# Optimization experiments

Measured on AMD Instinct MI355X. Metric: run time of the kernel, lower is better.

Reference implementation:

```python
import jax, jax.numpy as jnp
import numpy as np

NUM_EXPERTS = 8
HIDDEN = 1024
FFN = 2048
TOKENS = 2048


def setup_inputs() -> dict:
    key = jax.random.key(0)
    k_x, k_idx, k_w1, k_w2 = jax.random.split(key, 4)
    scale = 0.02
    x = jax.random.normal(k_x, (TOKENS, HIDDEN), dtype=jnp.float32)
    expert_indices = jax.random.randint(k_idx, (TOKENS,), 0, NUM_EXPERTS, dtype=jnp.int64)
    W1 = jax.random.normal(k_w1, (NUM_EXPERTS, HIDDEN, FFN), dtype=jnp.float32) * scale
    b1 = jnp.zeros((NUM_EXPERTS, FFN), dtype=jnp.float32)
    W2 = jax.random.normal(k_w2, (NUM_EXPERTS, FFN, HIDDEN), dtype=jnp.float32) * scale
    b2 = jnp.zeros((NUM_EXPERTS, HIDDEN), dtype=jnp.float32)
    return {"x": x, "expert_indices": expert_indices, "W1": W1, "b1": b1, "W2": W2, "b2": b2}


def reference(x, expert_indices, W1, b1, W2, b2):
    # Each token routed to one expert's MLP: Linear -> GELU(exact) -> Linear.
    # Dropout is identity in eval mode. Loop is over the small fixed expert set.
    out = jnp.zeros_like(x)
    for e in range(NUM_EXPERTS):
        h = jax.nn.gelu(x @ W1[e] + b1[e], approximate=False)  # [T, FFN]
        y = h @ W2[e] + b2[e]                                   # [T, H]
        mask = (expert_indices == e)[:, None]
        out = out + jnp.where(mask, y, 0.0)
    return out
```

## Files before the change

kernel.cpp:

```cpp
#include <hip/hip_runtime.h>

#define T_TOK 2048
#define HID   1024
#define FFN   2048
#define NEXP  8
#define MAX_SLOTS 40

typedef __attribute__((ext_vector_type(8))) short bf16x8;
typedef __attribute__((ext_vector_type(4))) float f32x4;

__device__ __forceinline__ short f2bf(float f) {
    unsigned u = __builtin_bit_cast(unsigned, f);
    u = (u + 0x7fffu + ((u >> 16) & 1u)) >> 16;
    return (short)u;
}

__device__ __forceinline__ float gelu_exact(float x) {
    return 0.5f * x * (1.0f + erff(x * 0.70710678118654752f));
}

__device__ __forceinline__ void async_cp16(const short* g, short* l) {
    __builtin_amdgcn_global_load_lds(
        (const __attribute__((address_space(1))) unsigned int*)g,
        (__attribute__((address_space(3))) unsigned int*)l, 16, 0, 0);
}

__global__ __launch_bounds__(256) void prep_kernel(
        const float* __restrict__ x, const int* __restrict__ idx,
        const float* __restrict__ b2,
        short* __restrict__ xb, float* __restrict__ out,
        int* __restrict__ offs, int* __restrict__ cnts,
        int* __restrict__ tokl,
        int* __restrict__ slot_e, int* __restrict__ slot_t0) {
    int bx = blockIdx.x;
    int tid = threadIdx.x;
    if (bx < 1024) {
        int i = (bx * 256 + tid) * 8;
        float4 v0 = *(const float4*)(x + i);
        float4 v1 = *(const float4*)(x + i + 4);
        bf16x8 r = {f2bf(v0.x), f2bf(v0.y), f2bf(v0.z), f2bf(v0.w),
                    f2bf(v1.x), f2bf(v1.y), f2bf(v1.z), f2bf(v1.w)};
        *(bf16x8*)(xb + i) = r;
    } else if (bx < 1024 + T_TOK) {
        int t = bx - 1024;
        int e = idx[t];
        ((float4*)(out + (size_t)t * HID))[tid] =
            ((const float4*)(b2 + (size_t)e * HID))[tid];
    } else {
        __shared__ int c[NEXP], cur[NEXP], o[NEXP];
        if (tid < NEXP) { c[tid] = 0; cur[tid] = 0; }
        __syncthreads();
        for (int t = tid; t < T_TOK; t += 256) atomicAdd(&c[idx[t]], 1);
        __syncthreads();
        if (tid == 0) {
            int s = 0;
            for (int e = 0; e < NEXP; e++) { o[e] = s; s += c[e]; }
            int ns = 0;
            for (int e = 0; e < NEXP; e++)
                for (int t0 = 0; t0 < c[e]; t0 += 64) {
                    slot_e[ns] = e; slot_t0[ns] = t0; ns++;
                }
            for (; ns < MAX_SLOTS; ns++) slot_e[ns] = -1;
        }
        __syncthreads();
        if (tid < NEXP) { offs[tid] = o[tid]; cnts[tid] = c[tid]; }
        for (int t = tid; t < T_TOK; t += 256) {
            int e = idx[t];
            int p = o[e] + atomicAdd(&cur[e], 1);
            tokl[p] = t;
        }
    }
}

__global__ __launch_bounds__(256) void wtrans_kernel(
        const float* __restrict__ W1, const float* __restrict__ W2,
        short* __restrict__ W1T, short* __restrict__ W2T) {
    int z = blockIdx.z;
    const float* W; short* WT; int K, N, e;
    if (z < NEXP) { W = W1; WT = W1T; K = HID; N = FFN; e = z; }
    else          { W = W2; WT = W2T; K = FFN; N = HID; e = z - NEXP; }
    int n0 = blockIdx.x * 64, k0 = blockIdx.y * 64;
    if (n0 >= N || k0 >= K) return;
    const float* We = W + (size_t)e * K * N;
    short* WTe = WT + (size_t)e * N * K;
    __shared__ short Ts[64][72];
    int tid = threadIdx.x;
#pragma unroll
    for (int i = 0; i < 4; i++) {
        int c = tid + i * 256;
        int k = c >> 4, n4 = (c & 15) * 4;
        float4 v = *(const float4*)(We + (size_t)(k0 + k) * N + n0 + n4);
        short s0 = f2bf(v.x), s1 = f2bf(v.y), s2 = f2bf(v.z), s3 = f2bf(v.w);
        int ck = k >> 3, kj = k & 7;
        Ts[n4 + 0][((ck ^ (((n4 + 0) >> 3) & 7)) << 3) + kj] = s0;
        Ts[n4 + 1][((ck ^ (((n4 + 1) >> 3) & 7)) << 3) + kj] = s1;
        Ts[n4 + 2][((ck ^ (((n4 + 2) >> 3) & 7)) << 3) + kj] = s2;
        Ts[n4 + 3][((ck ^ (((n4 + 3) >> 3) & 7)) << 3) + kj] = s3;
    }
    __syncthreads();
#pragma unroll
    for (int i = 0; i < 2; i++) {
        int c = tid + i * 256;
        int n = c >> 3, ck = c & 7;
        bf16x8 v = *(const bf16x8*)&Ts[n][(ck ^ ((n >> 3) & 7)) << 3];
        *(bf16x8*)(WTe + (size_t)(n0 + n) * K + k0 + ck * 8) = v;
    }
}

__global__ __launch_bounds__(256) void gemm1_kernel(
        const short* __restrict__ xb, const short* __restrict__ W1T,
        const float* __restrict__ b1,
        const int* __restrict__ offs, const int* __restrict__ cnts,
        const int* __restrict__ tokl,
        const int* __restrict__ slot_e, const int* __restrict__ slot_t0,
        short* __restrict__ hg) {
    int s = blockIdx.y;
    int e = slot_e[s];
    if (e < 0) return;
    int t0 = slot_t0[s];
    int count = cnts[e];
    int off = offs[e];
    int n0 = blockIdx.x * 64;

    __shared__ short As[64 * 32];
    __shared__ short Bs[64 * 32];
    __shared__ int stok[64];

    int tid = threadIdx.x;
    if (tid < 64) {
        int p = t0 + tid;
        stok[tid] = tokl[off + (p < count ? p : count - 1)];
    }
    __syncthreads();

    int w = tid >> 6, lane = tid & 63, l15 = lane & 15, quad = lane >> 4;
    int wm = (w >> 1) * 32, wn = (w & 1) * 32;

    int srow = w * 16 + (lane >> 2);
    int schunk = (lane & 3) * 8;
    const short* gA = xb + (size_t)stok[srow] * HID + schunk;
    const short* gB = W1T + (size_t)e * FFN * HID + (size_t)(n0 + srow) * HID + schunk;
    short* lA = &As[w * 16 * 32];
    short* lB = &Bs[w * 16 * 32];

    f32x4 acc[2][2];
#pragma unroll
    for (int i = 0; i < 2; i++)
#pragma unroll
        for (int j = 0; j < 2; j++) acc[i][j] = (f32x4){0.f, 0.f, 0.f, 0.f};

    for (int kt = 0; kt < HID / 32; kt++) {
        async_cp16(gA + kt * 32, lA);
        async_cp16(gB + kt * 32, lB);
        __syncthreads();
        bf16x8 a0 = *(const bf16x8*)&As[(wm + l15) * 32 + quad * 8];
        bf16x8 a1 = *(const bf16x8*)&As[(wm + 16 + l15) * 32 + quad * 8];
        bf16x8 b0 = *(const bf16x8*)&Bs[(wn + l15) * 32 + quad * 8];
        bf16x8 b1v = *(const bf16x8*)&Bs[(wn + 16 + l15) * 32 + quad * 8];
        acc[0][0] = __builtin_amdgcn_mfma_f32_16x16x32_bf16(a0, b0, acc[0][0], 0, 0, 0);
        acc[0][1] = __builtin_amdgcn_mfma_f32_16x16x32_bf16(a0, b1v, acc[0][1], 0, 0, 0);
        acc[1][0] = __builtin_amdgcn_mfma_f32_16x16x32_bf16(a1, b0, acc[1][0], 0, 0, 0);
        acc[1][1] = __builtin_amdgcn_mfma_f32_16x16x32_bf16(a1, b1v, acc[1][1], 0, 0, 0);
        __syncthreads();
    }

#pragma unroll
    for (int mt = 0; mt < 2; mt++) {
        int rbase = wm + mt * 16 + quad * 4;
#pragma unroll
        for (int nt = 0; nt < 2; nt++) {
            int coln = n0 + wn + nt * 16 + l15;
            float bb = b1[e * FFN + coln];
#pragma unroll
            for (int r = 0; r < 4; r++) {
                int p = t0 + rbase + r;
                if (p < count) {
                    float hv = gelu_exact(acc[mt][nt][r] + bb);
                    hg[(size_t)(off + p) * FFN + coln] = f2bf(hv);
                }
            }
        }
    }
}

__global__ __launch_bounds__(256) void gemm2_kernel(
        const short* __restrict__ hg, const short* __restrict__ W2T,
        const int* __restrict__ offs, const int* __restrict__ cnts,
        const int* __restrict__ tokl,
        const int* __restrict__ slot_e, const int* __restrict__ slot_t0,
        float* __restrict__ out) {
    int s = blockIdx.y;
    int e = slot_e[s];
    if (e < 0) return;
    int t0 = slot_t0[s];
    int ks = blockIdx.z;
    int count = cnts[e];
    int off = offs[e];
    int n0 = blockIdx.x * 64;
    int kbase = ks * (FFN / 4);

    __shared__ short As[64 * 32];
    __shared__ short Bs[64 * 32];

    int tid = threadIdx.x;
    int w = tid >> 6, lane = tid & 63, l15 = lane & 15, quad = lane >> 4;
    int wm = (w >> 1) * 32, wn = (w & 1) * 32;

    int srow = w * 16 + (lane >> 2);
    int schunk = (lane & 3) * 8;
    int grow = off + (t0 + srow < count ? t0 + srow : count - 1);
    const short* gA = hg + (size_t)grow * FFN + kbase + schunk;
    const short* gB = W2T + (size_t)e * HID * FFN + (size_t)(n0 + srow) * FFN + kbase + schunk;
    short* lA = &As[w * 16 * 32];
    short* lB = &Bs[w * 16 * 32];

    f32x4 acc[2][2];
#pragma unroll
    for (int i = 0; i < 2; i++)
#pragma unroll
        for (int j = 0; j < 2; j++) acc[i][j] = (f32x4){0.f, 0.f, 0.f, 0.f};

    for (int kt = 0; kt < FFN / 4 / 32; kt++) {
        async_cp16(gA + kt * 32, lA);
        async_cp16(gB + kt * 32, lB);
        __syncthreads();
        bf16x8 a0 = *(const bf16x8*)&As[(wm + l15) * 32 + quad * 8];
        bf16x8 a1 = *(const bf16x8*)&As[(wm + 16 + l15) * 32 + quad * 8];
        bf16x8 b0 = *(const bf16x8*)&Bs[(wn + l15) * 32 + quad * 8];
        bf16x8 b1v = *(const bf16x8*)&Bs[(wn + 16 + l15) * 32 + quad * 8];
        acc[0][0] = __builtin_amdgcn_mfma_f32_16x16x32_bf16(a0, b0, acc[0][0], 0, 0, 0);
        acc[0][1] = __builtin_amdgcn_mfma_f32_16x16x32_bf16(a0, b1v, acc[0][1], 0, 0, 0);
        acc[1][0] = __builtin_amdgcn_mfma_f32_16x16x32_bf16(a1, b0, acc[1][0], 0, 0, 0);
        acc[1][1] = __builtin_amdgcn_mfma_f32_16x16x32_bf16(a1, b1v, acc[1][1], 0, 0, 0);
        __syncthreads();
    }

#pragma unroll
    for (int mt = 0; mt < 2; mt++) {
        int rbase = wm + mt * 16 + quad * 4;
#pragma unroll
        for (int nt = 0; nt < 2; nt++) {
            int coln = n0 + wn + nt * 16 + l15;
#pragma unroll
            for (int r = 0; r < 4; r++) {
                int p = t0 + rbase + r;
                if (p < count) {
                    int tok = tokl[off + p];
                    atomicAdd(out + (size_t)tok * HID + coln, acc[mt][nt][r]);
                }
            }
        }
    }
}

extern "C" void kernel_launch(void* const* d_in, const int* in_sizes, int n_in,
                              void* d_out, int out_size, void* d_ws, size_t ws_size,
                              hipStream_t stream) {
    const float* x   = (const float*)d_in[0];
    const int*   idx = (const int*)d_in[1];
    const float* W1  = (const float*)d_in[2];
    const float* b1  = (const float*)d_in[3];
    const float* W2  = (const float*)d_in[4];
    const float* b2  = (const float*)d_in[5];
    float* out = (float*)d_out;

    const size_t META = 32768;
    int*   offs    = (int*)d_ws;
    int*   cnts    = offs + 8;
    int*   tokl    = offs + 16;
    int*   slot_e  = offs + 16 + T_TOK;
    int*   slot_t0 = slot_e + MAX_SLOTS;
    char*  base    = (char*)d_ws + META;
    short* xb  = (short*)base;
    short* hg  = (short*)(base + (size_t)T_TOK * HID * 2);
    short* W1T = (short*)(base + (size_t)T_TOK * HID * 2 + (size_t)T_TOK * FFN * 2);
    short* W2T = W1T + (size_t)NEXP * FFN * HID;

    prep_kernel<<<1024 + T_TOK + 1, 256, 0, stream>>>(
        x, idx, b2, xb, out, offs, cnts, tokl, slot_e, slot_t0);
    wtrans_kernel<<<dim3(32, 32, 16), 256, 0, stream>>>(W1, W2, W1T, W2T);

    gemm1_kernel<<<dim3(FFN / 64, MAX_SLOTS), 256, 0, stream>>>(
        xb, W1T, b1, offs, cnts, tokl, slot_e, slot_t0, hg);
    gemm2_kernel<<<dim3(HID / 64, MAX_SLOTS, 4), 256, 0, stream>>>(
        hg, W2T, offs, cnts, tokl, slot_e, slot_t0, out);
}
```

Baseline: 255.0 us.

## Fuse weight transpose into prep kernel and enlarge GEMM tiles with panel layout

The separate weight transpose kernel is folded into the prep kernel. It now writes W1/W2 as bf16 in a k-panel-blocked layout (64 k by 128 n panels), built with register transposes instead of LDS. Both GEMMs move to 64x128 tiles with a 64-wide k step, contiguous B-panel loads and an XOR-rotated A layout in LDS. GEMM2 uses 2 k-splits instead of 4. The goal is to cut launch count, barrier and load overhead per MFMA, and atomic traffic. The cost is fewer blocks in flight and higher register pressure.

```diff
diff --git a/kernel.cpp b/kernel.cpp
--- a/kernel.cpp
+++ b/kernel.cpp
@@ -25,24 +25,63 @@
         (__attribute__((address_space(3))) unsigned int*)l, 16, 0, 0);
 }
 
+__device__ __forceinline__ void wtrans_body(
+        const float* __restrict__ W, short* __restrict__ WT,
+        int K, int N, int e, int kblk, int nblk) {
+    int tid = threadIdx.x;
+    int w = tid >> 6, l = tid & 63;
+    int kb = kblk * 32 + w * 8;
+    int n4 = nblk * 256 + l * 4;
+    const float* src = W + (size_t)e * K * N + (size_t)kb * N + n4;
+    float4 v[8];
+#pragma unroll
+    for (int r = 0; r < 8; r++)
+        v[r] = *(const float4*)(src + (size_t)r * N);
+    int kpanel = kb >> 6;
+    int kc = (kb >> 3) & 7;
+    int npanel = n4 >> 7;
+    int n_in = n4 & 127;
+    int kpanels = K >> 6;
+    short* dst = WT + (size_t)e * K * N
+               + ((size_t)npanel * kpanels + kpanel) * 8192
+               + kc * 1024 + n_in * 8;
+#pragma unroll
+    for (int j = 0; j < 4; j++) {
+        bf16x8 o = {f2bf(((const float*)&v[0])[j]), f2bf(((const float*)&v[1])[j]),
+                    f2bf(((const float*)&v[2])[j]), f2bf(((const float*)&v[3])[j]),
+                    f2bf(((const float*)&v[4])[j]), f2bf(((const float*)&v[5])[j]),
+                    f2bf(((const float*)&v[6])[j]), f2bf(((const float*)&v[7])[j])};
+        *(bf16x8*)(dst + j * 8) = o;
+    }
+}
+
 __global__ __launch_bounds__(256) void prep_kernel(
         const float* __restrict__ x, const int* __restrict__ idx,
         const float* __restrict__ b2,
+        const float* __restrict__ W1, const float* __restrict__ W2,
         short* __restrict__ xb, float* __restrict__ out,
+        short* __restrict__ W1T, short* __restrict__ W2T,
         int* __restrict__ offs, int* __restrict__ cnts,
         int* __restrict__ tokl,
         int* __restrict__ slot_e, int* __restrict__ slot_t0) {
     int bx = blockIdx.x;
     int tid = threadIdx.x;
-    if (bx < 1024) {
-        int i = (bx * 256 + tid) * 8;
+    if (bx < 2048) {
+        int e = bx >> 8, rem = bx & 255;
+        wtrans_body(W1, W1T, HID, FFN, e, rem & 31, rem >> 5);
+    } else if (bx < 4096) {
+        int b = bx - 2048;
+        int e = b >> 8, rem = b & 255;
+        wtrans_body(W2, W2T, FFN, HID, e, rem & 63, rem >> 6);
+    } else if (bx < 5120) {
+        int i = ((bx - 4096) * 256 + tid) * 8;
         float4 v0 = *(const float4*)(x + i);
         float4 v1 = *(const float4*)(x + i + 4);
         bf16x8 r = {f2bf(v0.x), f2bf(v0.y), f2bf(v0.z), f2bf(v0.w),
                     f2bf(v1.x), f2bf(v1.y), f2bf(v1.z), f2bf(v1.w)};
         *(bf16x8*)(xb + i) = r;
-    } else if (bx < 1024 + T_TOK) {
-        int t = bx - 1024;
+    } else if (bx < 7168) {
+        int t = bx - 5120;
         int e = idx[t];
         ((float4*)(out + (size_t)t * HID))[tid] =
             ((const float4*)(b2 + (size_t)e * HID))[tid];
@@ -69,41 +108,6 @@
             int p = o[e] + atomicAdd(&cur[e], 1);
             tokl[p] = t;
         }
-    }
-}
-
-__global__ __launch_bounds__(256) void wtrans_kernel(
-        const float* __restrict__ W1, const float* __restrict__ W2,
-        short* __restrict__ W1T, short* __restrict__ W2T) {
-    int z = blockIdx.z;
-    const float* W; short* WT; int K, N, e;
-    if (z < NEXP) { W = W1; WT = W1T; K = HID; N = FFN; e = z; }
-    else          { W = W2; WT = W2T; K = FFN; N = HID; e = z - NEXP; }
-    int n0 = blockIdx.x * 64, k0 = blockIdx.y * 64;
-    if (n0 >= N || k0 >= K) return;
-    const float* We = W + (size_t)e * K * N;
-    short* WTe = WT + (size_t)e * N * K;
-    __shared__ short Ts[64][72];
-    int tid = threadIdx.x;
-#pragma unroll
-    for (int i = 0; i < 4; i++) {
-        int c = tid + i * 256;
-        int k = c >> 4, n4 = (c & 15) * 4;
-        float4 v = *(const float4*)(We + (size_t)(k0 + k) * N + n0 + n4);
-        short s0 = f2bf(v.x), s1 = f2bf(v.y), s2 = f2bf(v.z), s3 = f2bf(v.w);
-        int ck = k >> 3, kj = k & 7;
-        Ts[n4 + 0][((ck ^ (((n4 + 0) >> 3) & 7)) << 3) + kj] = s0;
-        Ts[n4 + 1][((ck ^ (((n4 + 1) >> 3) & 7)) << 3) + kj] = s1;
-        Ts[n4 + 2][((ck ^ (((n4 + 2) >> 3) & 7)) << 3) + kj] = s2;
-        Ts[n4 + 3][((ck ^ (((n4 + 3) >> 3) & 7)) << 3) + kj] = s3;
-    }
-    __syncthreads();
-#pragma unroll
-    for (int i = 0; i < 2; i++) {
-        int c = tid + i * 256;
-        int n = c >> 3, ck = c & 7;
-        bf16x8 v = *(const bf16x8*)&Ts[n][(ck ^ ((n >> 3) & 7)) << 3];
-        *(bf16x8*)(WTe + (size_t)(n0 + n) * K + k0 + ck * 8) = v;
     }
 }
 
@@ -117,13 +121,11 @@
     int s = blockIdx.y;
     int e = slot_e[s];
     if (e < 0) return;
-    int t0 = slot_t0[s];
-    int count = cnts[e];
-    int off = offs[e];
-    int n0 = blockIdx.x * 64;
-
-    __shared__ short As[64 * 32];
-    __shared__ short Bs[64 * 32];
+    int t0 = slot_t0[s], count = cnts[e], off = offs[e];
+    int n0 = blockIdx.x * 128;
+
+    __shared__ short As[64 * 64];
+    __shared__ short Bs[8 * 128 * 8];
     __shared__ int stok[64];
 
     int tid = threadIdx.x;
@@ -133,51 +135,79 @@
     }
     __syncthreads();
 
-    int w = tid >> 6, lane = tid & 63, l15 = lane & 15, quad = lane >> 4;
-    int wm = (w >> 1) * 32, wn = (w & 1) * 32;
-
-    int srow = w * 16 + (lane >> 2);
-    int schunk = (lane & 3) * 8;
-    const short* gA = xb + (size_t)stok[srow] * HID + schunk;
-    const short* gB = W1T + (size_t)e * FFN * HID + (size_t)(n0 + srow) * HID + schunk;
-    short* lA = &As[w * 16 * 32];
-    short* lB = &Bs[w * 16 * 32];
-
-    f32x4 acc[2][2];
+    int w = tid >> 6, l = tid & 63, l15 = l & 15, quad = l >> 4;
+    int wm = (w >> 1) * 32, wn = (w & 1) * 64;
+
+    int m0 = w * 16 + (l >> 3), m1 = m0 + 8;
+    int cs = l & 7;
+    int c0 = (cs - m0) & 7, c1 = (cs - m1) & 7;
+    const short* gA0 = xb + (size_t)stok[m0] * HID + c0 * 8;
+    const short* gA1 = xb + (size_t)stok[m1] * HID + c1 * 8;
+    short* lA0 = As + w * 1024 + l * 8;
+    short* lA1 = lA0 + 512;
+
+    const short* Bpan = W1T + (size_t)e * (FFN * HID)
+                      + (size_t)(n0 >> 7) * ((HID >> 6) * 8192);
+    int bo0 = (2 * w) * 1024 + l * 8;
+    int bo1 = bo0 + 1024;
+    int bo2 = bo0 + 512;
+    int bo3 = bo1 + 512;
+
+    f32x4 acc[2][4];
 #pragma unroll
     for (int i = 0; i < 2; i++)
 #pragma unroll
-        for (int j = 0; j < 2; j++) acc[i][j] = (f32x4){0.f, 0.f, 0.f, 0.f};
-
-    for (int kt = 0; kt < HID / 32; kt++) {
-        async_cp16(gA + kt * 32, lA);
-        async_cp16(gB + kt * 32, lB);
-        __syncthreads();
-        bf16x8 a0 = *(const bf16x8*)&As[(wm + l15) * 32 + quad * 8];
-        bf16x8 a1 = *(const bf16x8*)&As[(wm + 16 + l15) * 32 + quad * 8];
-        bf16x8 b0 = *(const bf16x8*)&Bs[(wn + l15) * 32 + quad * 8];
-        bf16x8 b1v = *(const bf16x8*)&Bs[(wn + 16 + l15) * 32 + quad * 8];
-        acc[0][0] = __builtin_amdgcn_mfma_f32_16x16x32_bf16(a0, b0, acc[0][0], 0, 0, 0);
-        acc[0][1] = __builtin_amdgcn_mfma_f32_16x16x32_bf16(a0, b1v, acc[0][1], 0, 0, 0);
-        acc[1][0] = __builtin_amdgcn_mfma_f32_16x16x32_bf16(a1, b0, acc[1][0], 0, 0, 0);
-        acc[1][1] = __builtin_amdgcn_mfma_f32_16x16x32_bf16(a1, b1v, acc[1][1], 0, 0, 0);
-        __syncthreads();
-    }
-
+        for (int j = 0; j < 4; j++) acc[i][j] = (f32x4){0.f, 0.f, 0.f, 0.f};
+
+    for (int kt = 0; kt < HID / 64; kt++) {
+        const short* bp = Bpan + kt * 8192;
+        async_cp16(gA0, lA0);
+        async_cp16(gA1, lA1);
+        async_cp16(bp + bo0, Bs + bo0);
+        async_cp16(bp + bo1, Bs + bo1);
+        async_cp16(bp + bo2, Bs + bo2);
+        async_cp16(bp + bo3, Bs + bo3);
+        gA0 += 64; gA1 += 64;
+        __syncthreads();
+        bf16x8 a[2][2], b[2][4];
+#pragma unroll
+        for (int kk = 0; kk < 2; kk++) {
+#pragma unroll
+            for (int mt = 0; mt < 2; mt++) {
+                int m = wm + mt * 16 + l15;
+                a[kk][mt] = *(const bf16x8*)&As[m * 64 + (((kk * 4 + quad) + m) & 7) * 8];
+            }
+#pragma unroll
+            for (int nt = 0; nt < 4; nt++) {
+                int n = wn + nt * 16 + l15;
+                b[kk][nt] = *(const bf16x8*)&Bs[(kk * 4 + quad) * 1024 + n * 8];
+            }
+        }
+#pragma unroll
+        for (int kk = 0; kk < 2; kk++)
+#pragma unroll
+            for (int mt = 0; mt < 2; mt++)
+#pragma unroll
+                for (int nt = 0; nt < 4; nt++)
+                    acc[mt][nt] = __builtin_amdgcn_mfma_f32_16x16x32_bf16(
+                        a[kk][mt], b[kk][nt], acc[mt][nt], 0, 0, 0);
+        __syncthreads();
+    }
+
+    const float* b1e = b1 + e * FFN + n0;
 #pragma unroll
     for (int mt = 0; mt < 2; mt++) {
         int rbase = wm + mt * 16 + quad * 4;
 #pragma unroll
-        for (int nt = 0; nt < 2; nt++) {
-            int coln = n0 + wn + nt * 16 + l15;
-            float bb = b1[e * FFN + coln];
+        for (int nt = 0; nt < 4; nt++) {
+            int coln = wn + nt * 16 + l15;
+            float bb = b1e[coln];
 #pragma unroll
             for (int r = 0; r < 4; r++) {
                 int p = t0 + rbase + r;
-                if (p < count) {
-                    float hv = gelu_exact(acc[mt][nt][r] + bb);
-                    hg[(size_t)(off + p) * FFN + coln] = f2bf(hv);
-                }
+                if (p < count)
+                    hg[(size_t)(off + p) * FFN + n0 + coln] =
+                        f2bf(gelu_exact(acc[mt][nt][r] + bb));
             }
         }
     }
@@ -192,46 +222,73 @@
     int s = blockIdx.y;
     int e = slot_e[s];
     if (e < 0) return;
-    int t0 = slot_t0[s];
+    int t0 = slot_t0[s], count = cnts[e], off = offs[e];
     int ks = blockIdx.z;
-    int count = cnts[e];
-    int off = offs[e];
-    int n0 = blockIdx.x * 64;
-    int kbase = ks * (FFN / 4);
-
-    __shared__ short As[64 * 32];
-    __shared__ short Bs[64 * 32];
+    int n0 = blockIdx.x * 128;
+
+    __shared__ short As[64 * 64];
+    __shared__ short Bs[8 * 128 * 8];
 
     int tid = threadIdx.x;
-    int w = tid >> 6, lane = tid & 63, l15 = lane & 15, quad = lane >> 4;
-    int wm = (w >> 1) * 32, wn = (w & 1) * 32;
-
-    int srow = w * 16 + (lane >> 2);
-    int schunk = (lane & 3) * 8;
-    int grow = off + (t0 + srow < count ? t0 + srow : count - 1);
-    const short* gA = hg + (size_t)grow * FFN + kbase + schunk;
-    const short* gB = W2T + (size_t)e * HID * FFN + (size_t)(n0 + srow) * FFN + kbase + schunk;
-    short* lA = &As[w * 16 * 32];
-    short* lB = &Bs[w * 16 * 32];
-
-    f32x4 acc[2][2];
+    int w = tid >> 6, l = tid & 63, l15 = l & 15, quad = l >> 4;
+    int wm = (w >> 1) * 32, wn = (w & 1) * 64;
+
+    int m0 = w * 16 + (l >> 3), m1 = m0 + 8;
+    int cs = l & 7;
+    int c0 = (cs - m0) & 7, c1 = (cs - m1) & 7;
+    int g0 = off + (t0 + m0 < count ? t0 + m0 : count - 1);
+    int g1 = off + (t0 + m1 < count ? t0 + m1 : count - 1);
+    const short* gA0 = hg + (size_t)g0 * FFN + ks * 1024 + c0 * 8;
+    const short* gA1 = hg + (size_t)g1 * FFN + ks * 1024 + c1 * 8;
+    short* lA0 = As + w * 1024 + l * 8;
+    short* lA1 = lA0 + 512;
+
+    const short* Bpan = W2T + (size_t)e * (FFN * HID)
+                      + (size_t)(n0 >> 7) * ((FFN >> 6) * 8192)
+                      + (size_t)ks * 16 * 8192;
+    int bo0 = (2 * w) * 1024 + l * 8;
+    int bo1 = bo0 + 1024;
+    int bo2 = bo0 + 512;
+    int bo3 = bo1 + 512;
+
+    f32x4 acc[2][4];
 #pragma unroll
     for (int i = 0; i < 2; i++)
 #pragma unroll
-        for (int j = 0; j < 2; j++) acc[i][j] = (f32x4){0.f, 0.f, 0.f, 0.f};
-
-    for (int kt = 0; kt < FFN / 4 / 32; kt++) {
-        async_cp16(gA + kt * 32, lA);
-        async_cp16(gB + kt * 32, lB);
-        __syncthreads();
-        bf16x8 a0 = *(const bf16x8*)&As[(wm + l15) * 32 + quad * 8];
-        bf16x8 a1 = *(const bf16x8*)&As[(wm + 16 + l15) * 32 + quad * 8];
-        bf16x8 b0 = *(const bf16x8*)&Bs[(wn + l15) * 32 + quad * 8];
-        bf16x8 b1v = *(const bf16x8*)&Bs[(wn + 16 + l15) * 32 + quad * 8];
-        acc[0][0] = __builtin_amdgcn_mfma_f32_16x16x32_bf16(a0, b0, acc[0][0], 0, 0, 0);
-        acc[0][1] = __builtin_amdgcn_mfma_f32_16x16x32_bf16(a0, b1v, acc[0][1], 0, 0, 0);
-        acc[1][0] = __builtin_amdgcn_mfma_f32_16x16x32_bf16(a1, b0, acc[1][0], 0, 0, 0);
-        acc[1][1] = __builtin_amdgcn_mfma_f32_16x16x32_bf16(a1, b1v, acc[1][1], 0, 0, 0);
+        for (int j = 0; j < 4; j++) acc[i][j] = (f32x4){0.f, 0.f, 0.f, 0.f};
+
+    for (int kt = 0; kt < 16; kt++) {
+        const short* bp = Bpan + kt * 8192;
+        async_cp16(gA0, lA0);
+        async_cp16(gA1, lA1);
+        async_cp16(bp + bo0, Bs + bo0);
+        async_cp16(bp + bo1, Bs + bo1);
+        async_cp16(bp + bo2, Bs + bo2);
+        async_cp16(bp + bo3, Bs + bo3);
+        gA0 += 64; gA1 += 64;
+        __syncthreads();
+        bf16x8 a[2][2], b[2][4];
+#pragma unroll
+        for (int kk = 0; kk < 2; kk++) {
+#pragma unroll
+            for (int mt = 0; mt < 2; mt++) {
+                int m = wm + mt * 16 + l15;
+                a[kk][mt] = *(const bf16x8*)&As[m * 64 + (((kk * 4 + quad) + m) & 7) * 8];
+            }
+#pragma unroll
+            for (int nt = 0; nt < 4; nt++) {
+                int n = wn + nt * 16 + l15;
+                b[kk][nt] = *(const bf16x8*)&Bs[(kk * 4 + quad) * 1024 + n * 8];
+            }
+        }
+#pragma unroll
+        for (int kk = 0; kk < 2; kk++)
+#pragma unroll
+            for (int mt = 0; mt < 2; mt++)
+#pragma unroll
+                for (int nt = 0; nt < 4; nt++)
+                    acc[mt][nt] = __builtin_amdgcn_mfma_f32_16x16x32_bf16(
+                        a[kk][mt], b[kk][nt], acc[mt][nt], 0, 0, 0);
         __syncthreads();
     }
 
@@ -239,7 +296,7 @@
     for (int mt = 0; mt < 2; mt++) {
         int rbase = wm + mt * 16 + quad * 4;
 #pragma unroll
-        for (int nt = 0; nt < 2; nt++) {
+        for (int nt = 0; nt < 4; nt++) {
             int coln = n0 + wn + nt * 16 + l15;
 #pragma unroll
             for (int r = 0; r < 4; r++) {
@@ -276,12 +333,12 @@
     short* W1T = (short*)(base + (size_t)T_TOK * HID * 2 + (size_t)T_TOK * FFN * 2);
     short* W2T = W1T + (size_t)NEXP * FFN * HID;
 
-    prep_kernel<<<1024 + T_TOK + 1, 256, 0, stream>>>(
-        x, idx, b2, xb, out, offs, cnts, tokl, slot_e, slot_t0);
-    wtrans_kernel<<<dim3(32, 32, 16), 256, 0, stream>>>(W1, W2, W1T, W2T);
-
-    gemm1_kernel<<<dim3(FFN / 64, MAX_SLOTS), 256, 0, stream>>>(
+    prep_kernel<<<7169, 256, 0, stream>>>(
+        x, idx, b2, W1, W2, xb, out, W1T, W2T,
+        offs, cnts, tokl, slot_e, slot_t0);
+
+    gemm1_kernel<<<dim3(FFN / 128, MAX_SLOTS), 256, 0, stream>>>(
         xb, W1T, b1, offs, cnts, tokl, slot_e, slot_t0, hg);
-    gemm2_kernel<<<dim3(HID / 64, MAX_SLOTS, 4), 256, 0, stream>>>(
+    gemm2_kernel<<<dim3(HID / 128, MAX_SLOTS, 2), 256, 0, stream>>>(
         hg, W2T, offs, cnts, tokl, slot_e, slot_t0, out);
 }
```

Result: faster. 224.6 us (-11.9%).
